# Kernel tuning notes

Hardware: AMD Instinct MI355X
Metric: run time of the kernel (lower is better)

## Reference

```python
import jax, jax.numpy as jnp
import numpy as np


def setup_inputs() -> dict:
    key = jax.random.key(0)
    B, S, D = 16, 1024, 384
    x = jax.random.normal(jax.random.fold_in(key, 0), (B, S, D), dtype=jnp.float32)
    # integer per-token durations in [0, 10); the layer rounds+casts anyway
    dimensions = jax.random.randint(jax.random.fold_in(key, 1), (B, S), 0, 10).astype(jnp.int32)
    return {"x": x, "dimensions": dimensions}


def reference(x, dimensions):
    # Faithful math of Expand.call: repeat each x[b, i, :] dimensions[b, i] times
    # along axis 1, left-packed, zero-padded to the max total length in the batch.
    dims = jnp.round(dimensions.astype(jnp.float32)).astype(jnp.int32)  # [B, S]
    totals = jnp.sum(dims, axis=1)                                      # [B]
    T = int(jnp.max(totals))  # output length (concrete; matches TF ragged .to_tensor())
    csum = jnp.cumsum(dims, axis=1)                                     # [B, S]
    t = jnp.arange(T, dtype=jnp.int32)                                  # [T]
    # source token index for each output position: first i with csum[i] > t
    idx = jax.vmap(lambda c: jnp.searchsorted(c, t, side='right'))(csum)  # [B, T]
    valid = (t[None, :] < totals[:, None])                              # [B, T]
    idx = jnp.minimum(idx, x.shape[1] - 1)                              # clamp padding positions
    out = jnp.take_along_axis(x, idx[..., None], axis=1)                # [B, T, D] gather
    return out * valid[..., None].astype(x.dtype)
```

## Files before the change

kernel.cpp:

```cpp
#include <hip/hip_runtime.h>
#include <hip/hip_bf16.h>


#define S_TOKENS 1024
#define B_BATCH 16
#define QVEC 96

typedef float f4 __attribute__((ext_vector_type(4)));

__global__ void prep_kernel(const int* __restrict__ dims, int* __restrict__ idx,
                            int T) {
    __shared__ int wsum[16];
    __shared__ int wexc[16];
    const int b    = blockIdx.x;
    const int tid  = threadIdx.x;
    const int lane = tid & 63;
    const int wid  = tid >> 6;

    const int v = dims[b * S_TOKENS + tid];
    int inc = v;
#pragma unroll
    for (int d = 1; d < 64; d <<= 1) {
        int u = __shfl_up(inc, d, 64);
        if (lane >= d) inc += u;
    }
    if (lane == 63) wsum[wid] = inc;
    __syncthreads();
    if (tid < 16) {
        int w = wsum[tid];
        int incw = w;
#pragma unroll
        for (int d = 1; d < 16; d <<= 1) {
            int u = __shfl_up(incw, d, 16);
            if (tid >= d) incw += u;
        }
        wexc[tid] = incw - w;
    }
    __syncthreads();

    const int end   = inc + wexc[wid];
    const int start = end - v;
    const int total = wexc[15] + wsum[15];

    int* __restrict__ idx_b = idx + b * T;
    const int src = b * S_TOKENS + tid;
    for (int t = start; t < end; ++t) idx_b[t] = src;
    for (int t = total + tid; t < T; t += S_TOKENS) idx_b[t] = -1;
}

__global__ void expand_kernel(const f4* __restrict__ x4,
                              const int* __restrict__ idx,
                              f4* __restrict__ out4,
                              int n4) {
    const int base = blockIdx.x * 512 + threadIdx.x;
#pragma unroll
    for (int half = 0; half < 2; ++half) {
        const int k = base + half * 256;
        if (k < n4) {
            int row = k / QVEC;
            int q   = k - row * QVEC;
            int src = idx[row];
            f4 val = (f4)(0.f, 0.f, 0.f, 0.f);
            if (src >= 0) val = x4[src * QVEC + q];
            __builtin_nontemporal_store(val, &out4[k]);
        }
    }
}

extern "C" void kernel_launch(void* const* d_in, const int* in_sizes, int n_in,
                              void* d_out, int out_size, void* d_ws, size_t ws_size,
                              hipStream_t stream) {
    const float* x    = (const float*)d_in[0];
    const int*   dims = (const int*)d_in[1];
    float*       out  = (float*)d_out;

    const int D = in_sizes[0] / in_sizes[1];
    const int T = out_size / (B_BATCH * D);

    int* idx = (int*)d_ws;

    prep_kernel<<<B_BATCH, S_TOKENS, 0, stream>>>(dims, idx, T);

    const int n4 = out_size / 4;
    const int grid = (n4 + 511) / 512;
    expand_kernel<<<grid, 256, 0, stream>>>((const f4*)x, idx, (f4*)out, n4);
}
```

Baseline: 152.3 us.

## Switch expand to per-token scatter: load each row once, write repeats

The prep kernel now writes only the per-batch inclusive cumsum, with no per-output-row index table. The expand kernel assigns one wavefront per source token. It loads the 384-float row into registers once and writes it rep times to consecutive output rows. Extra blocks zero-fill the padding tail for each batch. This drops the idx write/read pass and the redundant re-reads of x per output row, at the cost of load imbalance across tokens with different repeat counts, idle wavefronts for zero-duration tokens, and the loss of nontemporal stores.

```diff
diff --git a/kernel.cpp b/kernel.cpp
--- a/kernel.cpp
+++ b/kernel.cpp
@@ -5,11 +5,12 @@
 #define S_TOKENS 1024
 #define B_BATCH 16
 #define QVEC 96
+#define TOK_BLOCKS (B_BATCH * S_TOKENS / 4)
+#define PAD_BLOCKS 64
 
 typedef float f4 __attribute__((ext_vector_type(4)));
 
-__global__ void prep_kernel(const int* __restrict__ dims, int* __restrict__ idx,
-                            int T) {
+__global__ void scan_kernel(const int* __restrict__ dims, int* __restrict__ csum) {
     __shared__ int wsum[16];
     __shared__ int wexc[16];
     const int b    = blockIdx.x;
@@ -37,33 +38,45 @@
         wexc[tid] = incw - w;
     }
     __syncthreads();
-
-    const int end   = inc + wexc[wid];
-    const int start = end - v;
-    const int total = wexc[15] + wsum[15];
-
-    int* __restrict__ idx_b = idx + b * T;
-    const int src = b * S_TOKENS + tid;
-    for (int t = start; t < end; ++t) idx_b[t] = src;
-    for (int t = total + tid; t < T; t += S_TOKENS) idx_b[t] = -1;
+    csum[b * S_TOKENS + tid] = inc + wexc[wid];
 }
 
 __global__ void expand_kernel(const f4* __restrict__ x4,
-                              const int* __restrict__ idx,
-                              f4* __restrict__ out4,
-                              int n4) {
-    const int base = blockIdx.x * 512 + threadIdx.x;
-#pragma unroll
-    for (int half = 0; half < 2; ++half) {
-        const int k = base + half * 256;
-        if (k < n4) {
-            int row = k / QVEC;
-            int q   = k - row * QVEC;
-            int src = idx[row];
-            f4 val = (f4)(0.f, 0.f, 0.f, 0.f);
-            if (src >= 0) val = x4[src * QVEC + q];
-            __builtin_nontemporal_store(val, &out4[k]);
+                              const int* __restrict__ csum,
+                              f4* __restrict__ out4, int T) {
+    const int blk = blockIdx.x;
+    if (blk < TOK_BLOCKS) {
+        const int wid   = threadIdx.x >> 6;
+        const int lane  = threadIdx.x & 63;
+        const int token = blk * 4 + wid;
+        const int b     = token >> 10;
+        const int i     = token & (S_TOKENS - 1);
+        const int* __restrict__ c = csum + b * S_TOKENS;
+        const int end   = c[i];
+        const int start = (i == 0) ? 0 : c[i - 1];
+        const int rep   = end - start;
+        if (rep <= 0) return;
+
+        const f4* __restrict__ row = x4 + (size_t)(b * S_TOKENS + i) * QVEC;
+        f4 v0 = row[lane];
+        f4 v1 = (f4)(0.f, 0.f, 0.f, 0.f);
+        if (lane < 32) v1 = row[64 + lane];
+
+        f4* dst = out4 + ((size_t)b * T + start) * QVEC;
+        for (int r = 0; r < rep; ++r, dst += QVEC) {
+            dst[lane] = v0;
+            if (lane < 32) dst[64 + lane] = v1;
         }
+    } else {
+        const int p   = blk - TOK_BLOCKS;
+        const int b   = p >> 2;
+        const int sub = p & 3;
+        const int total = csum[b * S_TOKENS + S_TOKENS - 1];
+        const int n = (T - total) * QVEC;
+        f4* __restrict__ dst = out4 + ((size_t)b * T + total) * QVEC;
+        const f4 z = (f4)(0.f, 0.f, 0.f, 0.f);
+        for (int j = sub * 256 + threadIdx.x; j < n; j += 4 * 256)
+            dst[j] = z;
     }
 }
 
@@ -77,11 +90,10 @@
     const int D = in_sizes[0] / in_sizes[1];
     const int T = out_size / (B_BATCH * D);
 
-    int* idx = (int*)d_ws;
+    int* csum = (int*)d_ws;
 
-    prep_kernel<<<B_BATCH, S_TOKENS, 0, stream>>>(dims, idx, T);
+    scan_kernel<<<B_BATCH, S_TOKENS, 0, stream>>>(dims, csum);
 
-    const int n4 = out_size / 4;
-    const int grid = (n4 + 511) / 512;
-    expand_kernel<<<grid, 256, 0, stream>>>((const f4*)x, idx, (f4*)out, n4);
+    expand_kernel<<<TOK_BLOCKS + PAD_BLOCKS, 256, 0, stream>>>(
+        (const f4*)x, csum, (f4*)out, T);
 }
```

New measurement: 141.7 us. -7.0%, faster.
